# Kernel tuning notes

Hardware: AMD Instinct MI355X
Metric: run time of the kernel (lower is better)

## Reference

```python
import jax, jax.numpy as jnp
from jax import lax
import numpy as np

B, T, D, H, W = 256, 1024, 4, 64, 128

# Tsit5 Butcher tableau
C2, C3, C4, C5 = 0.161, 0.327, 0.9, 0.9800255409045097
A21 = 0.161
A31, A32 = -0.008480655492356989, 0.335480655492357
A41, A42, A43 = 2.8971530571054935, -6.359448489975075, 4.3622954328695815
A51, A52, A53, A54 = 5.325864828439257, -11.748883564062828, 7.4955393428898365, -0.09249506636175525
A61, A62, A63, A64, A65 = 5.86145544294642, -12.92096931784711, 8.159367898576159, -0.071584973281401, -0.028269050394068383
BW1, BW2, BW3, BW4, BW5, BW6 = 0.09646076681806523, 0.01, 0.4798896504144996, 1.379008574103742, -3.290069515436081, 2.324710524099774


def setup_inputs() -> dict:
    key = jax.random.key(0)
    ks = jax.random.split(key, 20)
    f32 = jnp.float32
    ts = jnp.arange(T, dtype=f32)
    coef = lambda k: 0.1 * jax.random.normal(k, (B, T - 1, D), f32)
    g = lambda k, shp, fan: jax.random.normal(k, shp, f32) / np.sqrt(fan)
    return {
        'ts': ts,
        'coef_d': coef(ks[0]), 'coef_c': coef(ks[1]),
        'coef_b': coef(ks[2]), 'coef_a': coef(ks[3]),
        # initial MLP: D -> W -> W -> H (softplus hidden, identity final)
        'W0': g(ks[4], (W, D), D), 'b0': jnp.zeros((W,), f32),
        'W1': g(ks[5], (W, W), W), 'b1': jnp.zeros((W,), f32),
        'W2': g(ks[6], (H, W), W), 'b2': jnp.zeros((H,), f32),
        # vector-field MLP: H -> W -> W -> H*D (softplus hidden, tanh final)
        'F0': g(ks[7], (W, H), H), 'g0': jnp.zeros((W,), f32),
        'F1': g(ks[8], (W, W), W), 'g1': jnp.zeros((W,), f32),
        'F2': g(ks[9], (H * D, W), W), 'g2': jnp.zeros((H * D,), f32),
        # readout: H -> 3
        'L': g(ks[10], (3, H), H), 'lb': jnp.zeros((3,), f32),
        'evolving_out': 1,
    }


def reference(ts, coef_d, coef_c, coef_b, coef_a,
              W0, b0, W1, b1, W2, b2,
              F0, g0, F1, g1, F2, g2, L, lb, evolving_out):
    sp = jax.nn.softplus

    def vf(y, dx):  # y: (B,H), dx: (B,D) -> f(y) @ dX/dt : (B,H)
        h1 = sp(y @ F0.T + g0)
        h2 = sp(h1 @ F1.T + g1)
        f = jnp.tanh(h2 @ F2.T + g2).reshape(-1, H, D)
        return jnp.einsum('bhd,bd->bh', f, dx)

    def step(y, inp):
        dt, cb, cc, cd = inp  # dt scalar; cb/cc/cd: (B,D) cubic coeffs of interval
        dx = lambda frac: cb + frac * (2.0 * cc + 3.0 * frac * cd)
        k1 = vf(y, dx(0.0))
        k2 = vf(y + dt * (A21 * k1), dx(C2 * dt))
        k3 = vf(y + dt * (A31 * k1 + A32 * k2), dx(C3 * dt))
        k4 = vf(y + dt * (A41 * k1 + A42 * k2 + A43 * k3), dx(C4 * dt))
        k5 = vf(y + dt * (A51 * k1 + A52 * k2 + A53 * k3 + A54 * k4), dx(C5 * dt))
        k6 = vf(y + dt * (A61 * k1 + A62 * k2 + A63 * k3 + A64 * k4 + A65 * k5), dx(dt))
        ynew = y + dt * (BW1 * k1 + BW2 * k2 + BW3 * k3 + BW4 * k4 + BW5 * k5 + BW6 * k6)
        return ynew, ynew

    # y0 = initial_mlp(X(t0)); X(t0) = coef_a at first interval (frac = 0)
    x0 = coef_a[:, 0]  # (B,D)
    h1 = sp(x0 @ W0.T + b0)
    h2 = sp(h1 @ W1.T + b1)
    y0 = h2 @ W2.T + b2  # (B,H)

    dts = ts[1:] - ts[:-1]  # (T-1,)
    xs = (dts, coef_b.transpose(1, 0, 2), coef_c.transpose(1, 0, 2), coef_d.transpose(1, 0, 2))
    ylast, ys = lax.scan(step, y0, xs)  # ys: (T-1,B,H)

    if evolving_out:
        ys_all = jnp.concatenate([y0[None], ys], axis=0)  # (T,B,H)
        return jnp.einsum('tbh,oh->bto', ys_all, L) + lb  # (B,T,3)
    return ylast @ L.T + lb  # (B,3)
```

## Files before the change

### kernel.cpp

```cpp
#include <hip/hip_runtime.h>

namespace {

constexpr int NB    = 256;
constexpr int NT    = 1024;
constexpr int NSTEP = NT - 1;
constexpr int D = 4, H = 64, W = 128;

constexpr float cAT[6][5] = {
    {0.f, 0.f, 0.f, 0.f, 0.f},
    {0.161f, 0.f, 0.f, 0.f, 0.f},
    {-0.008480655492356989f, 0.335480655492357f, 0.f, 0.f, 0.f},
    {2.8971530571054935f, -6.359448489975075f, 4.3622954328695815f, 0.f, 0.f},
    {5.325864828439257f, -11.748883564062828f, 7.4955393428898365f, -0.09249506636175525f, 0.f},
    {5.86145544294642f, -12.92096931784711f, 8.159367898576159f, -0.071584973281401f, -0.028269050394068383f}};
constexpr float cFR[6] = {0.0f, 0.161f, 0.327f, 0.9f, 0.9800255409045097f, 1.0f};
constexpr float cBW[6] = {0.09646076681806523f, 0.01f, 0.4798896504144996f,
                          1.379008574103742f, -3.290069515436081f, 2.324710524099774f};

__device__ __forceinline__ float softplus_f(float x) {
    float e = __expf(-fabsf(x));
    return fmaxf(x, 0.0f) + __logf(1.0f + e);
}
__device__ __forceinline__ float tanh_f(float x) {
    float e = __expf(2.0f * x);
    return 1.0f - __fdividef(2.0f, 1.0f + e);
}

template <int CTRL>
__device__ __forceinline__ float dppmv(float x) {
    return __int_as_float(__builtin_amdgcn_mov_dpp(__float_as_int(x), CTRL, 0xF, 0xF, true));
}

__device__ __forceinline__ int pY(int i)  { return (i >> 4) * 20 + (i & 15); }
__device__ __forceinline__ int p1i(int i) { return (i >> 5) * 36 + (i & 31); }
__device__ __forceinline__ int p2i(int i) { return (i >> 6) * 72 + (i & 63); }

__global__ __launch_bounds__(512, 2)
void cde_kernel(const float* __restrict__ ts,
                const float* __restrict__ coef_d,
                const float* __restrict__ coef_c,
                const float* __restrict__ coef_b,
                const float* __restrict__ coef_a,
                const float* __restrict__ W0, const float* __restrict__ b0,
                const float* __restrict__ W1, const float* __restrict__ b1,
                const float* __restrict__ W2, const float* __restrict__ b2,
                const float* __restrict__ F0, const float* __restrict__ g0,
                const float* __restrict__ F1, const float* __restrict__ g1,
                const float* __restrict__ F2, const float* __restrict__ g2,
                const float* __restrict__ Lm, const float* __restrict__ lb,
                float* __restrict__ out)
{
    const int b    = blockIdx.x;
    const int tid  = threadIdx.x;

    const int j12  = tid >> 2;
    const int q12  = tid & 3;
    const int j3   = tid >> 1;
    const int q3   = tid & 1;
    const int d3   = j3 & 3;
    const int hown = tid >> 3;

    __shared__ __align__(16) float s_ys[80];
    __shared__ __align__(16) float s_h1[144];
    __shared__ __align__(16) float s_h2[136];

    float wA[16];
    float wB[32];
    float wC[64];
    #pragma unroll
    for (int i = 0; i < 16; i += 4) {
        float4 v = *reinterpret_cast<const float4*>(F0 + j12 * H + q12 * 16 + i);
        wA[i+0]=v.x; wA[i+1]=v.y; wA[i+2]=v.z; wA[i+3]=v.w;
    }
    #pragma unroll
    for (int i = 0; i < 32; i += 4) {
        float4 v = *reinterpret_cast<const float4*>(F1 + j12 * W + q12 * 32 + i);
        wB[i+0]=v.x; wB[i+1]=v.y; wB[i+2]=v.z; wB[i+3]=v.w;
    }
    #pragma unroll
    for (int i = 0; i < 64; i += 4) {
        float4 v = *reinterpret_cast<const float4*>(F2 + j3 * W + q3 * 64 + i);
        wC[i+0]=v.x; wC[i+1]=v.y; wC[i+2]=v.z; wC[i+3]=v.w;
    }
    const float g0r = g0[j12];
    const float g1r = g1[j12];
    const float g2r = g2[j3];
    const float L0r = Lm[0*H + (tid & 63)];
    const float L1r = Lm[1*H + (tid & 63)];
    const float L2r = Lm[2*H + (tid & 63)];
    const float lb0 = lb[0], lb1 = lb[1], lb2 = lb[2];

    const float* pA  = s_ys + q12 * 20;
    const float* pB  = s_h1 + q12 * 36;
    const float* pC  = s_h2 + q3  * 72;
    float* pw1 = s_h1 + p1i(j12);
    float* pw2 = s_h2 + p2i(j12);
    float* pwy = s_ys + pY(hown);

    if (tid < W) {
        const float4 x0 = *reinterpret_cast<const float4*>(coef_a + (size_t)b * NSTEP * D);
        const float4 w  = *reinterpret_cast<const float4*>(W0 + tid * D);
        s_h1[p1i(tid)] = softplus_f(w.x*x0.x + w.y*x0.y + w.z*x0.z + w.w*x0.w + b0[tid]);
    }
    __syncthreads();
    if (tid < W) {
        float a = b1[tid];
        #pragma unroll
        for (int blk = 0; blk < 4; ++blk)
            #pragma unroll
            for (int i = 0; i < 8; ++i) {
                float4 wv = *reinterpret_cast<const float4*>(W1 + tid * W + blk * 32 + 4 * i);
                float4 hv = *reinterpret_cast<const float4*>(s_h1 + blk * 36 + 4 * i);
                a += wv.x*hv.x + wv.y*hv.y + wv.z*hv.z + wv.w*hv.w;
            }
        s_h2[p2i(tid)] = softplus_f(a);
    }
    __syncthreads();
    if (tid < H) {
        float a = b2[tid];
        #pragma unroll
        for (int blk = 0; blk < 2; ++blk)
            #pragma unroll
            for (int i = 0; i < 16; ++i) {
                float4 wv = *reinterpret_cast<const float4*>(W2 + tid * W + blk * 64 + 4 * i);
                float4 hv = *reinterpret_cast<const float4*>(s_h2 + blk * 72 + 4 * i);
                a += wv.x*hv.x + wv.y*hv.y + wv.z*hv.z + wv.w*hv.w;
            }
        s_ys[pY(tid)] = a;
    }
    __syncthreads();

    float y = s_ys[pY(hown)];

    auto project = [&](int tslot) {
        if (tid < 64) {
            float yv = s_ys[pY(tid)];
            float p0 = yv * L0r, p1 = yv * L1r, p2 = yv * L2r;
            #pragma unroll
            for (int off = 32; off >= 1; off >>= 1) {
                p0 += __shfl_xor(p0, off);
                p1 += __shfl_xor(p1, off);
                p2 += __shfl_xor(p2, off);
            }
            if (tid == 0) {
                float* dst = out + ((size_t)b * NT + tslot) * 3;
                dst[0] = p0 + lb0; dst[1] = p1 + lb1; dst[2] = p2 + lb2;
            }
        }
    };
    project(0);

    const float* cb_p = coef_b + (size_t)b * NSTEP * D + d3;
    const float* cc_p = coef_c + (size_t)b * NSTEP * D + d3;
    const float* cd_p = coef_d + (size_t)b * NSTEP * D + d3;

    for (int t = 0; t < NSTEP; ++t) {
        const float cbd = cb_p[t * D];
        const float ccd = cc_p[t * D];
        const float cdd = cd_p[t * D];
        const float dtv = ts[t + 1] - ts[t];

        float k[6];

        #pragma unroll
        for (int s = 0; s < 6; ++s) {
            float4 h0 = *reinterpret_cast<const float4*>(pA + 0);
            float4 h1 = *reinterpret_cast<const float4*>(pA + 4);
            float4 h2 = *reinterpret_cast<const float4*>(pA + 8);
            float4 h3 = *reinterpret_cast<const float4*>(pA + 12);
            float a1  = wA[0]*h0.x + wA[1]*h0.y + wA[2]*h0.z + wA[3]*h0.w
                      + wA[4]*h1.x + wA[5]*h1.y + wA[6]*h1.z + wA[7]*h1.w;
            float a1b = wA[8]*h2.x + wA[9]*h2.y + wA[10]*h2.z + wA[11]*h2.w
                      + wA[12]*h3.x + wA[13]*h3.y + wA[14]*h3.z + wA[15]*h3.w;
            float a1s = a1 + a1b;
            a1s += dppmv<0xB1>(a1s);
            a1s += dppmv<0x4E>(a1s);
            if (q12 == 0) *pw1 = softplus_f(a1s + g0r);
            __syncthreads();

            float a2 = 0.f, a2b = 0.f;
            #pragma unroll
            for (int c = 0; c < 8; c += 2) {
                float4 u0 = *reinterpret_cast<const float4*>(pB + 4 * c);
                float4 u1 = *reinterpret_cast<const float4*>(pB + 4 * c + 4);
                a2  += wB[4*c+0]*u0.x + wB[4*c+1]*u0.y + wB[4*c+2]*u0.z + wB[4*c+3]*u0.w;
                a2b += wB[4*c+4]*u1.x + wB[4*c+5]*u1.y + wB[4*c+6]*u1.z + wB[4*c+7]*u1.w;
            }
            float a2s = a2 + a2b;
            a2s += dppmv<0xB1>(a2s);
            a2s += dppmv<0x4E>(a2s);
            if (q12 == 0) *pw2 = softplus_f(a2s + g1r);
            __syncthreads();

            float a3 = 0.f, a3b = 0.f;
            #pragma unroll
            for (int c = 0; c < 16; c += 2) {
                float4 u0 = *reinterpret_cast<const float4*>(pC + 4 * c);
                float4 u1 = *reinterpret_cast<const float4*>(pC + 4 * c + 4);
                a3  += wC[4*c+0]*u0.x + wC[4*c+1]*u0.y + wC[4*c+2]*u0.z + wC[4*c+3]*u0.w;
                a3b += wC[4*c+4]*u1.x + wC[4*c+5]*u1.y + wC[4*c+6]*u1.z + wC[4*c+7]*u1.w;
            }
            float a3s = a3 + a3b;
            a3s += dppmv<0xB1>(a3s);
            const float f = tanh_f(a3s + g2r);

            const float frac = cFR[s] * dtv;
            const float dxd  = fmaf(frac, fmaf(3.0f * frac, cdd, 2.0f * ccd), cbd);
            float v = f * dxd;
            v += dppmv<0x4E>(v);
            v += dppmv<0x141>(v);
            k[s] = v;

            float ysn;
            if (s < 5) {
                float acc = 0.f;
                #pragma unroll
                for (int i = 0; i <= s; ++i) acc = fmaf(cAT[s+1][i], k[i], acc);
                ysn = fmaf(dtv, acc, y);
            } else {
                float acc = 0.f;
                #pragma unroll
                for (int i = 0; i < 6; ++i) acc = fmaf(cBW[i], k[i], acc);
                ysn = fmaf(dtv, acc, y);
            }
            if ((tid & 7) == 0) *pwy = ysn;
            __syncthreads();
        }

        y = s_ys[pY(hown)];

        project(t + 1);
    }
}

}

extern "C" void kernel_launch(void* const* d_in, const int* in_sizes, int n_in,
                              void* d_out, int out_size, void* d_ws, size_t ws_size,
                              hipStream_t stream) {
    const float* ts     = (const float*)d_in[0];
    const float* coef_d = (const float*)d_in[1];
    const float* coef_c = (const float*)d_in[2];
    const float* coef_b = (const float*)d_in[3];
    const float* coef_a = (const float*)d_in[4];
    const float* W0 = (const float*)d_in[5];
    const float* b0 = (const float*)d_in[6];
    const float* W1 = (const float*)d_in[7];
    const float* b1 = (const float*)d_in[8];
    const float* W2 = (const float*)d_in[9];
    const float* b2 = (const float*)d_in[10];
    const float* F0 = (const float*)d_in[11];
    const float* g0 = (const float*)d_in[12];
    const float* F1 = (const float*)d_in[13];
    const float* g1 = (const float*)d_in[14];
    const float* F2 = (const float*)d_in[15];
    const float* g2 = (const float*)d_in[16];
    const float* Lm = (const float*)d_in[17];
    const float* lb = (const float*)d_in[18];
    float* out = (float*)d_out;

    hipLaunchKernelGGL(cde_kernel, dim3(NB), dim3(512), 0, stream,
                       ts, coef_d, coef_c, coef_b, coef_a,
                       W0, b0, W1, b1, W2, b2,
                       F0, g0, F1, g1, F2, g2, Lm, lb, out);
}
```

Before: 6.908 ms.

## Repartition vector-field MLP across lanes with packed FMA and transpose-style DPP reduction

Reassigns work so that each thread computes partial dot products for four output neurons over a short slice of the input, instead of one neuron over a long slice. Each thread now reads fewer shared-memory vectors per layer. Partial sums are combined with a DPP butterfly that acts as a transpose-reduce over 16 lanes. The inner products use packed two-wide float FMAs, and the shared buffers are re-padded to match the new access pattern. In the last layer all four D components are handled in one thread, and the CDE coefficients are loaded as float4. This removes the cross-lane reduction over D, but adds redundant tanh work and more select/DPP instructions.

```diff
diff --git a/kernel.cpp b/kernel.cpp
--- a/kernel.cpp
+++ b/kernel.cpp
@@ -6,6 +6,8 @@
 constexpr int NT    = 1024;
 constexpr int NSTEP = NT - 1;
 constexpr int D = 4, H = 64, W = 128;
+
+typedef float v2f __attribute__((ext_vector_type(2)));
 
 constexpr float cAT[6][5] = {
     {0.f, 0.f, 0.f, 0.f, 0.f},
@@ -18,6 +20,8 @@
 constexpr float cBW[6] = {0.09646076681806523f, 0.01f, 0.4798896504144996f,
                           1.379008574103742f, -3.290069515436081f, 2.324710524099774f};
 
+#define PINF(x) asm volatile("" : "+v"(x))
+
 __device__ __forceinline__ float softplus_f(float x) {
     float e = __expf(-fabsf(x));
     return fmaxf(x, 0.0f) + __logf(1.0f + e);
@@ -32,9 +36,8 @@
     return __int_as_float(__builtin_amdgcn_mov_dpp(__float_as_int(x), CTRL, 0xF, 0xF, true));
 }
 
-__device__ __forceinline__ int pY(int i)  { return (i >> 4) * 20 + (i & 15); }
-__device__ __forceinline__ int p1i(int i) { return (i >> 5) * 36 + (i & 31); }
-__device__ __forceinline__ int p2i(int i) { return (i >> 6) * 72 + (i & 63); }
+__device__ __forceinline__ int p1m(int i) { return i + ((i >> 3) << 2); }
+__device__ __forceinline__ int p2m(int i) { return i + ((i >> 4) << 2); }
 
 __global__ __launch_bounds__(512, 2)
 void cde_kernel(const float* __restrict__ ts,
@@ -51,91 +54,126 @@
                 const float* __restrict__ Lm, const float* __restrict__ lb,
                 float* __restrict__ out)
 {
-    const int b    = blockIdx.x;
-    const int tid  = threadIdx.x;
-
-    const int j12  = tid >> 2;
-    const int q12  = tid & 3;
-    const int j3   = tid >> 1;
-    const int q3   = tid & 1;
-    const int d3   = j3 & 3;
-    const int hown = tid >> 3;
-
-    __shared__ __align__(16) float s_ys[80];
-    __shared__ __align__(16) float s_h1[144];
-    __shared__ __align__(16) float s_h2[136];
-
-    float wA[16];
-    float wB[32];
-    float wC[64];
-    #pragma unroll
-    for (int i = 0; i < 16; i += 4) {
-        float4 v = *reinterpret_cast<const float4*>(F0 + j12 * H + q12 * 16 + i);
-        wA[i+0]=v.x; wA[i+1]=v.y; wA[i+2]=v.z; wA[i+3]=v.w;
-    }
-    #pragma unroll
-    for (int i = 0; i < 32; i += 4) {
-        float4 v = *reinterpret_cast<const float4*>(F1 + j12 * W + q12 * 32 + i);
-        wB[i+0]=v.x; wB[i+1]=v.y; wB[i+2]=v.z; wB[i+3]=v.w;
-    }
-    #pragma unroll
-    for (int i = 0; i < 64; i += 4) {
-        float4 v = *reinterpret_cast<const float4*>(F2 + j3 * W + q3 * 64 + i);
-        wC[i+0]=v.x; wC[i+1]=v.y; wC[i+2]=v.z; wC[i+3]=v.w;
-    }
-    const float g0r = g0[j12];
-    const float g1r = g1[j12];
-    const float g2r = g2[j3];
-    const float L0r = Lm[0*H + (tid & 63)];
-    const float L1r = Lm[1*H + (tid & 63)];
-    const float L2r = Lm[2*H + (tid & 63)];
+    const int b   = blockIdx.x;
+    const int tid = threadIdx.x;
+
+    const int q1 = tid & 15;
+    const int gO = tid >> 4;
+    const int q3 = tid & 7;
+    const int g3 = tid >> 3;
+    const bool wr12 = (q1 < 4);
+    const bool wry  = (q3 == 0);
+    const bool pb0  = (tid & 1) != 0;
+    const bool pb1  = (tid & 2) != 0;
+
+    __shared__ __align__(16) float s_ys[64];
+    __shared__ __align__(16) float s_h1[192];
+    __shared__ __align__(16) float s_h2[160];
+
+    v2f wA2[8];
+    v2f wB2[16];
+    v2f wC2[32];
+    #pragma unroll
+    for (int j = 0; j < 4; ++j) {
+        float4 v = *reinterpret_cast<const float4*>(F0 + (4*gO + j) * H + 4*q1);
+        wA2[2*j]   = v2f{v.x, v.y};
+        wA2[2*j+1] = v2f{v.z, v.w};
+    }
+    #pragma unroll
+    for (int j = 0; j < 4; ++j)
+        #pragma unroll
+        for (int m = 0; m < 2; ++m) {
+            float4 v = *reinterpret_cast<const float4*>(F1 + (4*gO + j) * W + 8*q1 + 4*m);
+            wB2[4*j + 2*m]     = v2f{v.x, v.y};
+            wB2[4*j + 2*m + 1] = v2f{v.z, v.w};
+        }
+    #pragma unroll
+    for (int j = 0; j < 4; ++j)
+        #pragma unroll
+        for (int m = 0; m < 4; ++m) {
+            float4 v = *reinterpret_cast<const float4*>(F2 + (4*g3 + j) * W + 16*q3 + 4*m);
+            wC2[8*j + 2*m]     = v2f{v.x, v.y};
+            wC2[8*j + 2*m + 1] = v2f{v.z, v.w};
+        }
+    float g0w = g0[4*gO + (tid & 3)];
+    float g1w = g1[4*gO + (tid & 3)];
+    float g2v0 = g2[4*g3 + 0], g2v1 = g2[4*g3 + 1], g2v2 = g2[4*g3 + 2], g2v3 = g2[4*g3 + 3];
+    float L0r = Lm[0*H + (tid & 63)];
+    float L1r = Lm[1*H + (tid & 63)];
+    float L2r = Lm[2*H + (tid & 63)];
     const float lb0 = lb[0], lb1 = lb[1], lb2 = lb[2];
 
-    const float* pA  = s_ys + q12 * 20;
-    const float* pB  = s_h1 + q12 * 36;
-    const float* pC  = s_h2 + q3  * 72;
-    float* pw1 = s_h1 + p1i(j12);
-    float* pw2 = s_h2 + p2i(j12);
-    float* pwy = s_ys + pY(hown);
+    #pragma unroll
+    for (int i = 0; i < 8;  ++i) PINF(wA2[i]);
+    #pragma unroll
+    for (int i = 0; i < 16; ++i) PINF(wB2[i]);
+    #pragma unroll
+    for (int i = 0; i < 32; ++i) PINF(wC2[i]);
+    PINF(g0w); PINF(g1w); PINF(g2v0); PINF(g2v1); PINF(g2v2); PINF(g2v3);
+    PINF(L0r); PINF(L1r); PINF(L2r);
+
+    const float* pA = s_ys + 4*q1;
+    const float* pB = s_h1 + 12*q1;
+    const float* pC = s_h2 + 20*q3;
+    float* pw1 = s_h1 + p1m(4*gO + (tid & 3));
+    float* pw2 = s_h2 + p2m(4*gO + (tid & 3));
+    float* pwy = s_ys + g3;
+
+    auto reduce16 = [&](float v0, float v1, float v2, float v3) -> float {
+        v0 += dppmv<0x128>(v0); v1 += dppmv<0x128>(v1);
+        v2 += dppmv<0x128>(v2); v3 += dppmv<0x128>(v3);
+        v0 += dppmv<0x141>(v0); v1 += dppmv<0x141>(v1);
+        v2 += dppmv<0x141>(v2); v3 += dppmv<0x141>(v3);
+        float a  = pb0 ? v1 : v0;
+        float as = pb0 ? v0 : v1;
+        a += dppmv<0xB1>(as);
+        float c  = pb0 ? v3 : v2;
+        float cs = pb0 ? v2 : v3;
+        c += dppmv<0xB1>(cs);
+        float keep = pb1 ? c : a;
+        float send = pb1 ? a : c;
+        return keep + dppmv<0x4E>(send);
+    };
 
     if (tid < W) {
         const float4 x0 = *reinterpret_cast<const float4*>(coef_a + (size_t)b * NSTEP * D);
         const float4 w  = *reinterpret_cast<const float4*>(W0 + tid * D);
-        s_h1[p1i(tid)] = softplus_f(w.x*x0.x + w.y*x0.y + w.z*x0.z + w.w*x0.w + b0[tid]);
+        s_h1[p1m(tid)] = softplus_f(w.x*x0.x + w.y*x0.y + w.z*x0.z + w.w*x0.w + b0[tid]);
     }
     __syncthreads();
     if (tid < W) {
         float a = b1[tid];
         #pragma unroll
-        for (int blk = 0; blk < 4; ++blk)
-            #pragma unroll
-            for (int i = 0; i < 8; ++i) {
-                float4 wv = *reinterpret_cast<const float4*>(W1 + tid * W + blk * 32 + 4 * i);
-                float4 hv = *reinterpret_cast<const float4*>(s_h1 + blk * 36 + 4 * i);
-                a += wv.x*hv.x + wv.y*hv.y + wv.z*hv.z + wv.w*hv.w;
-            }
-        s_h2[p2i(tid)] = softplus_f(a);
+        for (int c = 0; c < 16; ++c) {
+            float4 wv0 = *reinterpret_cast<const float4*>(W1 + tid * W + 8*c);
+            float4 wv1 = *reinterpret_cast<const float4*>(W1 + tid * W + 8*c + 4);
+            float4 hv0 = *reinterpret_cast<const float4*>(s_h1 + 12*c);
+            float4 hv1 = *reinterpret_cast<const float4*>(s_h1 + 12*c + 4);
+            a += wv0.x*hv0.x + wv0.y*hv0.y + wv0.z*hv0.z + wv0.w*hv0.w
+               + wv1.x*hv1.x + wv1.y*hv1.y + wv1.z*hv1.z + wv1.w*hv1.w;
+        }
+        s_h2[p2m(tid)] = softplus_f(a);
     }
     __syncthreads();
     if (tid < H) {
         float a = b2[tid];
         #pragma unroll
-        for (int blk = 0; blk < 2; ++blk)
+        for (int c = 0; c < 8; ++c)
             #pragma unroll
-            for (int i = 0; i < 16; ++i) {
-                float4 wv = *reinterpret_cast<const float4*>(W2 + tid * W + blk * 64 + 4 * i);
-                float4 hv = *reinterpret_cast<const float4*>(s_h2 + blk * 72 + 4 * i);
+            for (int m = 0; m < 4; ++m) {
+                float4 wv = *reinterpret_cast<const float4*>(W2 + tid * W + 16*c + 4*m);
+                float4 hv = *reinterpret_cast<const float4*>(s_h2 + 20*c + 4*m);
                 a += wv.x*hv.x + wv.y*hv.y + wv.z*hv.z + wv.w*hv.w;
             }
-        s_ys[pY(tid)] = a;
+        s_ys[tid] = a;
     }
     __syncthreads();
 
-    float y = s_ys[pY(hown)];
+    float y = *pwy;
 
     auto project = [&](int tslot) {
         if (tid < 64) {
-            float yv = s_ys[pY(tid)];
+            float yv = s_ys[tid];
             float p0 = yv * L0r, p1 = yv * L1r, p2 = yv * L2r;
             #pragma unroll
             for (int off = 32; off >= 1; off >>= 1) {
@@ -151,85 +189,107 @@
     };
     project(0);
 
-    const float* cb_p = coef_b + (size_t)b * NSTEP * D + d3;
-    const float* cc_p = coef_c + (size_t)b * NSTEP * D + d3;
-    const float* cd_p = coef_d + (size_t)b * NSTEP * D + d3;
+    const float* cb_p = coef_b + (size_t)b * NSTEP * D;
+    const float* cc_p = coef_c + (size_t)b * NSTEP * D;
+    const float* cd_p = coef_d + (size_t)b * NSTEP * D;
 
     for (int t = 0; t < NSTEP; ++t) {
-        const float cbd = cb_p[t * D];
-        const float ccd = cc_p[t * D];
-        const float cdd = cd_p[t * D];
+        const float4 cb4 = *reinterpret_cast<const float4*>(cb_p + (size_t)t * D);
+        const float4 cc4 = *reinterpret_cast<const float4*>(cc_p + (size_t)t * D);
+        const float4 cd4 = *reinterpret_cast<const float4*>(cd_p + (size_t)t * D);
         const float dtv = ts[t + 1] - ts[t];
 
         float k[6];
 
         #pragma unroll
         for (int s = 0; s < 6; ++s) {
-            float4 h0 = *reinterpret_cast<const float4*>(pA + 0);
-            float4 h1 = *reinterpret_cast<const float4*>(pA + 4);
-            float4 h2 = *reinterpret_cast<const float4*>(pA + 8);
-            float4 h3 = *reinterpret_cast<const float4*>(pA + 12);
-            float a1  = wA[0]*h0.x + wA[1]*h0.y + wA[2]*h0.z + wA[3]*h0.w
-                      + wA[4]*h1.x + wA[5]*h1.y + wA[6]*h1.z + wA[7]*h1.w;
-            float a1b = wA[8]*h2.x + wA[9]*h2.y + wA[10]*h2.z + wA[11]*h2.w
-                      + wA[12]*h3.x + wA[13]*h3.y + wA[14]*h3.z + wA[15]*h3.w;
-            float a1s = a1 + a1b;
-            a1s += dppmv<0xB1>(a1s);
-            a1s += dppmv<0x4E>(a1s);
-            if (q12 == 0) *pw1 = softplus_f(a1s + g0r);
+            {
+                float4 hv = *reinterpret_cast<const float4*>(pA);
+                v2f h01 = v2f{hv.x, hv.y}, h23 = v2f{hv.z, hv.w};
+                v2f a0 = __builtin_elementwise_fma(wA2[1], h23, wA2[0] * h01);
+                v2f a1 = __builtin_elementwise_fma(wA2[3], h23, wA2[2] * h01);
+                v2f a2 = __builtin_elementwise_fma(wA2[5], h23, wA2[4] * h01);
+                v2f a3 = __builtin_elementwise_fma(wA2[7], h23, wA2[6] * h01);
+                float c = reduce16(a0.x + a0.y, a1.x + a1.y, a2.x + a2.y, a3.x + a3.y);
+                float sp = softplus_f(c + g0w);
+                if (wr12) *pw1 = sp;
+            }
             __syncthreads();
 
-            float a2 = 0.f, a2b = 0.f;
-            #pragma unroll
-            for (int c = 0; c < 8; c += 2) {
-                float4 u0 = *reinterpret_cast<const float4*>(pB + 4 * c);
-                float4 u1 = *reinterpret_cast<const float4*>(pB + 4 * c + 4);
-                a2  += wB[4*c+0]*u0.x + wB[4*c+1]*u0.y + wB[4*c+2]*u0.z + wB[4*c+3]*u0.w;
-                a2b += wB[4*c+4]*u1.x + wB[4*c+5]*u1.y + wB[4*c+6]*u1.z + wB[4*c+7]*u1.w;
-            }
-            float a2s = a2 + a2b;
-            a2s += dppmv<0xB1>(a2s);
-            a2s += dppmv<0x4E>(a2s);
-            if (q12 == 0) *pw2 = softplus_f(a2s + g1r);
+            {
+                float4 u0 = *reinterpret_cast<const float4*>(pB);
+                float4 u1 = *reinterpret_cast<const float4*>(pB + 4);
+                v2f h0 = v2f{u0.x, u0.y}, h1 = v2f{u0.z, u0.w};
+                v2f h2 = v2f{u1.x, u1.y}, h3 = v2f{u1.z, u1.w};
+                v2f a0 = wB2[0]*h0, a1 = wB2[4]*h0, a2 = wB2[8]*h0, a3 = wB2[12]*h0;
+                a0 = __builtin_elementwise_fma(wB2[1],  h1, a0);
+                a1 = __builtin_elementwise_fma(wB2[5],  h1, a1);
+                a2 = __builtin_elementwise_fma(wB2[9],  h1, a2);
+                a3 = __builtin_elementwise_fma(wB2[13], h1, a3);
+                a0 = __builtin_elementwise_fma(wB2[2],  h2, a0);
+                a1 = __builtin_elementwise_fma(wB2[6],  h2, a1);
+                a2 = __builtin_elementwise_fma(wB2[10], h2, a2);
+                a3 = __builtin_elementwise_fma(wB2[14], h2, a3);
+                a0 = __builtin_elementwise_fma(wB2[3],  h3, a0);
+                a1 = __builtin_elementwise_fma(wB2[7],  h3, a1);
+                a2 = __builtin_elementwise_fma(wB2[11], h3, a2);
+                a3 = __builtin_elementwise_fma(wB2[15], h3, a3);
+                float c = reduce16(a0.x + a0.y, a1.x + a1.y, a2.x + a2.y, a3.x + a3.y);
+                float sp = softplus_f(c + g1w);
+                if (wr12) *pw2 = sp;
+            }
             __syncthreads();
 
-            float a3 = 0.f, a3b = 0.f;
-            #pragma unroll
-            for (int c = 0; c < 16; c += 2) {
-                float4 u0 = *reinterpret_cast<const float4*>(pC + 4 * c);
-                float4 u1 = *reinterpret_cast<const float4*>(pC + 4 * c + 4);
-                a3  += wC[4*c+0]*u0.x + wC[4*c+1]*u0.y + wC[4*c+2]*u0.z + wC[4*c+3]*u0.w;
-                a3b += wC[4*c+4]*u1.x + wC[4*c+5]*u1.y + wC[4*c+6]*u1.z + wC[4*c+7]*u1.w;
-            }
-            float a3s = a3 + a3b;
-            a3s += dppmv<0xB1>(a3s);
-            const float f = tanh_f(a3s + g2r);
-
-            const float frac = cFR[s] * dtv;
-            const float dxd  = fmaf(frac, fmaf(3.0f * frac, cdd, 2.0f * ccd), cbd);
-            float v = f * dxd;
-            v += dppmv<0x4E>(v);
-            v += dppmv<0x141>(v);
-            k[s] = v;
-
-            float ysn;
-            if (s < 5) {
-                float acc = 0.f;
+            {
+                v2f a0 = v2f{0.f, 0.f}, a1 = a0, a2 = a0, a3 = a0;
                 #pragma unroll
-                for (int i = 0; i <= s; ++i) acc = fmaf(cAT[s+1][i], k[i], acc);
-                ysn = fmaf(dtv, acc, y);
-            } else {
-                float acc = 0.f;
-                #pragma unroll
-                for (int i = 0; i < 6; ++i) acc = fmaf(cBW[i], k[i], acc);
-                ysn = fmaf(dtv, acc, y);
-            }
-            if ((tid & 7) == 0) *pwy = ysn;
+                for (int m = 0; m < 4; ++m) {
+                    float4 u = *reinterpret_cast<const float4*>(pC + 4*m);
+                    v2f hlo = v2f{u.x, u.y}, hhi = v2f{u.z, u.w};
+                    a0 = __builtin_elementwise_fma(wC2[2*m],      hlo, a0);
+                    a0 = __builtin_elementwise_fma(wC2[2*m+1],    hhi, a0);
+                    a1 = __builtin_elementwise_fma(wC2[8+2*m],    hlo, a1);
+                    a1 = __builtin_elementwise_fma(wC2[8+2*m+1],  hhi, a1);
+                    a2 = __builtin_elementwise_fma(wC2[16+2*m],   hlo, a2);
+                    a2 = __builtin_elementwise_fma(wC2[16+2*m+1], hhi, a2);
+                    a3 = __builtin_elementwise_fma(wC2[24+2*m],   hlo, a3);
+                    a3 = __builtin_elementwise_fma(wC2[24+2*m+1], hhi, a3);
+                }
+                float v0 = a0.x + a0.y, v1 = a1.x + a1.y, v2 = a2.x + a2.y, v3 = a3.x + a3.y;
+                v0 += dppmv<0xB1>(v0); v1 += dppmv<0xB1>(v1); v2 += dppmv<0xB1>(v2); v3 += dppmv<0xB1>(v3);
+                v0 += dppmv<0x4E>(v0); v1 += dppmv<0x4E>(v1); v2 += dppmv<0x4E>(v2); v3 += dppmv<0x4E>(v3);
+                v0 += dppmv<0x141>(v0); v1 += dppmv<0x141>(v1); v2 += dppmv<0x141>(v2); v3 += dppmv<0x141>(v3);
+
+                const float f0 = tanh_f(v0 + g2v0);
+                const float f1 = tanh_f(v1 + g2v1);
+                const float f2 = tanh_f(v2 + g2v2);
+                const float f3 = tanh_f(v3 + g2v3);
+
+                const float frac = cFR[s] * dtv;
+                const float dx0 = fmaf(frac, fmaf(3.0f*frac, cd4.x, 2.0f*cc4.x), cb4.x);
+                const float dx1 = fmaf(frac, fmaf(3.0f*frac, cd4.y, 2.0f*cc4.y), cb4.y);
+                const float dx2 = fmaf(frac, fmaf(3.0f*frac, cd4.z, 2.0f*cc4.z), cb4.z);
+                const float dx3 = fmaf(frac, fmaf(3.0f*frac, cd4.w, 2.0f*cc4.w), cb4.w);
+                k[s] = fmaf(f0, dx0, fmaf(f1, dx1, fmaf(f2, dx2, f3 * dx3)));
+
+                float ysn;
+                if (s < 5) {
+                    float acc = 0.f;
+                    #pragma unroll
+                    for (int i = 0; i <= s; ++i) acc = fmaf(cAT[s+1][i], k[i], acc);
+                    ysn = fmaf(dtv, acc, y);
+                } else {
+                    float acc = 0.f;
+                    #pragma unroll
+                    for (int i = 0; i < 6; ++i) acc = fmaf(cBW[i], k[i], acc);
+                    ysn = fmaf(dtv, acc, y);
+                }
+                if (wry) *pwy = ysn;
+            }
             __syncthreads();
         }
 
-        y = s_ys[pY(hown)];
-
+        y = *pwy;
         project(t + 1);
     }
 }
```

Result: slower. 7.807 ms (+13.0%).

## Compute two output rows per thread in layers 2 and 3 to reuse shared loads

Applied to the files above, without the earlier changes.

Layers 2 and 3 of the vector-field MLP are remapped so each thread computes partial dot products for two output neurons over a shorter slice of the input. Each float4 read from shared memory is then used twice, which cuts LDS traffic per FMA. The cost is extra DPP reduction steps and a different lane-to-dimension mapping for the dX contraction, which now sums duplicate partials scaled by 0.5. Register count per thread stays about the same.

```diff
diff --git a/kernel.cpp b/kernel.cpp
--- a/kernel.cpp
+++ b/kernel.cpp
@@ -56,47 +56,53 @@
 
     const int j12  = tid >> 2;
     const int q12  = tid & 3;
-    const int j3   = tid >> 1;
-    const int q3   = tid & 1;
-    const int d3   = j3 & 3;
-    const int hown = tid >> 3;
+    const int og   = tid >> 3;
+    const int q2   = tid & 7;
+    const int grp  = tid >> 2;
+    const int qc   = tid & 3;
+    const int g3   = tid >> 3;
+    const int dsel = ((tid >> 2) & 1) * 2 + (tid & 1);
 
     __shared__ __align__(16) float s_ys[80];
     __shared__ __align__(16) float s_h1[144];
     __shared__ __align__(16) float s_h2[136];
 
     float wA[16];
-    float wB[32];
-    float wC[64];
+    float wB0[16], wB1[16];
+    float wC0[32], wC1[32];
     #pragma unroll
     for (int i = 0; i < 16; i += 4) {
         float4 v = *reinterpret_cast<const float4*>(F0 + j12 * H + q12 * 16 + i);
         wA[i+0]=v.x; wA[i+1]=v.y; wA[i+2]=v.z; wA[i+3]=v.w;
     }
     #pragma unroll
+    for (int i = 0; i < 16; i += 4) {
+        float4 v0 = *reinterpret_cast<const float4*>(F1 + (2*og)     * W + q2 * 16 + i);
+        float4 v1 = *reinterpret_cast<const float4*>(F1 + (2*og + 1) * W + q2 * 16 + i);
+        wB0[i+0]=v0.x; wB0[i+1]=v0.y; wB0[i+2]=v0.z; wB0[i+3]=v0.w;
+        wB1[i+0]=v1.x; wB1[i+1]=v1.y; wB1[i+2]=v1.z; wB1[i+3]=v1.w;
+    }
+    #pragma unroll
     for (int i = 0; i < 32; i += 4) {
-        float4 v = *reinterpret_cast<const float4*>(F1 + j12 * W + q12 * 32 + i);
-        wB[i+0]=v.x; wB[i+1]=v.y; wB[i+2]=v.z; wB[i+3]=v.w;
-    }
-    #pragma unroll
-    for (int i = 0; i < 64; i += 4) {
-        float4 v = *reinterpret_cast<const float4*>(F2 + j3 * W + q3 * 64 + i);
-        wC[i+0]=v.x; wC[i+1]=v.y; wC[i+2]=v.z; wC[i+3]=v.w;
+        float4 v0 = *reinterpret_cast<const float4*>(F2 + (2*grp)     * W + qc * 32 + i);
+        float4 v1 = *reinterpret_cast<const float4*>(F2 + (2*grp + 1) * W + qc * 32 + i);
+        wC0[i+0]=v0.x; wC0[i+1]=v0.y; wC0[i+2]=v0.z; wC0[i+3]=v0.w;
+        wC1[i+0]=v1.x; wC1[i+1]=v1.y; wC1[i+2]=v1.z; wC1[i+3]=v1.w;
     }
     const float g0r = g0[j12];
-    const float g1r = g1[j12];
-    const float g2r = g2[j3];
+    const float g1s = g1[2*og  + (q2  & 1)];
+    const float g2s = g2[2*grp + (tid & 1)];
     const float L0r = Lm[0*H + (tid & 63)];
     const float L1r = Lm[1*H + (tid & 63)];
     const float L2r = Lm[2*H + (tid & 63)];
     const float lb0 = lb[0], lb1 = lb[1], lb2 = lb[2];
 
-    const float* pA  = s_ys + q12 * 20;
-    const float* pB  = s_h1 + q12 * 36;
-    const float* pC  = s_h2 + q3  * 72;
+    const float* pA = s_ys + q12 * 20;
+    const float* pB = s_h1 + (q2 >> 1) * 36 + (q2 & 1) * 16;
+    const float* pC = s_h2 + (qc >> 1) * 72 + (qc & 1) * 32;
     float* pw1 = s_h1 + p1i(j12);
-    float* pw2 = s_h2 + p2i(j12);
-    float* pwy = s_ys + pY(hown);
+    float* pw2 = s_h2 + p2i(2*og + (q2 & 1));
+    float* pwy = s_ys + pY(g3);
 
     if (tid < W) {
         const float4 x0 = *reinterpret_cast<const float4*>(coef_a + (size_t)b * NSTEP * D);
@@ -131,7 +137,7 @@
     }
     __syncthreads();
 
-    float y = s_ys[pY(hown)];
+    float y = s_ys[pY(g3)];
 
     auto project = [&](int tslot) {
         if (tid < 64) {
@@ -151,85 +157,95 @@
     };
     project(0);
 
-    const float* cb_p = coef_b + (size_t)b * NSTEP * D + d3;
-    const float* cc_p = coef_c + (size_t)b * NSTEP * D + d3;
-    const float* cd_p = coef_d + (size_t)b * NSTEP * D + d3;
+    const float* cb_pl = coef_b + (size_t)b * NSTEP * D + dsel;
+    const float* cc_pl = coef_c + (size_t)b * NSTEP * D + dsel;
+    const float* cd_pl = coef_d + (size_t)b * NSTEP * D + dsel;
 
     for (int t = 0; t < NSTEP; ++t) {
-        const float cbd = cb_p[t * D];
-        const float ccd = cc_p[t * D];
-        const float cdd = cd_p[t * D];
+        const float cbd = cb_pl[(size_t)t * D];
+        const float ccd = cc_pl[(size_t)t * D];
+        const float cdd = cd_pl[(size_t)t * D];
         const float dtv = ts[t + 1] - ts[t];
 
         float k[6];
 
         #pragma unroll
         for (int s = 0; s < 6; ++s) {
-            float4 h0 = *reinterpret_cast<const float4*>(pA + 0);
-            float4 h1 = *reinterpret_cast<const float4*>(pA + 4);
-            float4 h2 = *reinterpret_cast<const float4*>(pA + 8);
-            float4 h3 = *reinterpret_cast<const float4*>(pA + 12);
-            float a1  = wA[0]*h0.x + wA[1]*h0.y + wA[2]*h0.z + wA[3]*h0.w
-                      + wA[4]*h1.x + wA[5]*h1.y + wA[6]*h1.z + wA[7]*h1.w;
-            float a1b = wA[8]*h2.x + wA[9]*h2.y + wA[10]*h2.z + wA[11]*h2.w
-                      + wA[12]*h3.x + wA[13]*h3.y + wA[14]*h3.z + wA[15]*h3.w;
-            float a1s = a1 + a1b;
-            a1s += dppmv<0xB1>(a1s);
-            a1s += dppmv<0x4E>(a1s);
-            if (q12 == 0) *pw1 = softplus_f(a1s + g0r);
+            {
+                float4 h0 = *reinterpret_cast<const float4*>(pA + 0);
+                float4 h1 = *reinterpret_cast<const float4*>(pA + 4);
+                float4 h2 = *reinterpret_cast<const float4*>(pA + 8);
+                float4 h3 = *reinterpret_cast<const float4*>(pA + 12);
+                float a1  = wA[0]*h0.x + wA[1]*h0.y + wA[2]*h0.z + wA[3]*h0.w
+                          + wA[4]*h1.x + wA[5]*h1.y + wA[6]*h1.z + wA[7]*h1.w;
+                float a1b = wA[8]*h2.x + wA[9]*h2.y + wA[10]*h2.z + wA[11]*h2.w
+                          + wA[12]*h3.x + wA[13]*h3.y + wA[14]*h3.z + wA[15]*h3.w;
+                float a1s = a1 + a1b;
+                a1s += dppmv<0xB1>(a1s);
+                a1s += dppmv<0x4E>(a1s);
+                if (q12 == 0) *pw1 = softplus_f(a1s + g0r);
+            }
             __syncthreads();
 
-            float a2 = 0.f, a2b = 0.f;
-            #pragma unroll
-            for (int c = 0; c < 8; c += 2) {
-                float4 u0 = *reinterpret_cast<const float4*>(pB + 4 * c);
-                float4 u1 = *reinterpret_cast<const float4*>(pB + 4 * c + 4);
-                a2  += wB[4*c+0]*u0.x + wB[4*c+1]*u0.y + wB[4*c+2]*u0.z + wB[4*c+3]*u0.w;
-                a2b += wB[4*c+4]*u1.x + wB[4*c+5]*u1.y + wB[4*c+6]*u1.z + wB[4*c+7]*u1.w;
-            }
-            float a2s = a2 + a2b;
-            a2s += dppmv<0xB1>(a2s);
-            a2s += dppmv<0x4E>(a2s);
-            if (q12 == 0) *pw2 = softplus_f(a2s + g1r);
+            {
+                float4 u0 = *reinterpret_cast<const float4*>(pB + 0);
+                float4 u1 = *reinterpret_cast<const float4*>(pB + 4);
+                float4 u2 = *reinterpret_cast<const float4*>(pB + 8);
+                float4 u3 = *reinterpret_cast<const float4*>(pB + 12);
+                float p0 = wB0[0]*u0.x + wB0[1]*u0.y + wB0[2]*u0.z + wB0[3]*u0.w
+                         + wB0[4]*u1.x + wB0[5]*u1.y + wB0[6]*u1.z + wB0[7]*u1.w
+                         + wB0[8]*u2.x + wB0[9]*u2.y + wB0[10]*u2.z + wB0[11]*u2.w
+                         + wB0[12]*u3.x + wB0[13]*u3.y + wB0[14]*u3.z + wB0[15]*u3.w;
+                float p1 = wB1[0]*u0.x + wB1[1]*u0.y + wB1[2]*u0.z + wB1[3]*u0.w
+                         + wB1[4]*u1.x + wB1[5]*u1.y + wB1[6]*u1.z + wB1[7]*u1.w
+                         + wB1[8]*u2.x + wB1[9]*u2.y + wB1[10]*u2.z + wB1[11]*u2.w
+                         + wB1[12]*u3.x + wB1[13]*u3.y + wB1[14]*u3.z + wB1[15]*u3.w;
+                p0 += dppmv<0xB1>(p0); p1 += dppmv<0xB1>(p1);
+                p0 += dppmv<0x4E>(p0); p1 += dppmv<0x4E>(p1);
+                p0 += dppmv<0x141>(p0); p1 += dppmv<0x141>(p1);
+                float spv = softplus_f(((q2 & 1) ? p1 : p0) + g1s);
+                if (q2 < 2) *pw2 = spv;
+            }
             __syncthreads();
 
-            float a3 = 0.f, a3b = 0.f;
-            #pragma unroll
-            for (int c = 0; c < 16; c += 2) {
-                float4 u0 = *reinterpret_cast<const float4*>(pC + 4 * c);
-                float4 u1 = *reinterpret_cast<const float4*>(pC + 4 * c + 4);
-                a3  += wC[4*c+0]*u0.x + wC[4*c+1]*u0.y + wC[4*c+2]*u0.z + wC[4*c+3]*u0.w;
-                a3b += wC[4*c+4]*u1.x + wC[4*c+5]*u1.y + wC[4*c+6]*u1.z + wC[4*c+7]*u1.w;
-            }
-            float a3s = a3 + a3b;
-            a3s += dppmv<0xB1>(a3s);
-            const float f = tanh_f(a3s + g2r);
-
-            const float frac = cFR[s] * dtv;
-            const float dxd  = fmaf(frac, fmaf(3.0f * frac, cdd, 2.0f * ccd), cbd);
-            float v = f * dxd;
-            v += dppmv<0x4E>(v);
-            v += dppmv<0x141>(v);
-            k[s] = v;
-
-            float ysn;
-            if (s < 5) {
-                float acc = 0.f;
+            {
+                float p0 = 0.f, p1 = 0.f;
                 #pragma unroll
-                for (int i = 0; i <= s; ++i) acc = fmaf(cAT[s+1][i], k[i], acc);
-                ysn = fmaf(dtv, acc, y);
-            } else {
-                float acc = 0.f;
-                #pragma unroll
-                for (int i = 0; i < 6; ++i) acc = fmaf(cBW[i], k[i], acc);
-                ysn = fmaf(dtv, acc, y);
-            }
-            if ((tid & 7) == 0) *pwy = ysn;
+                for (int m = 0; m < 8; ++m) {
+                    float4 u = *reinterpret_cast<const float4*>(pC + 4*m);
+                    p0 += wC0[4*m+0]*u.x + wC0[4*m+1]*u.y + wC0[4*m+2]*u.z + wC0[4*m+3]*u.w;
+                    p1 += wC1[4*m+0]*u.x + wC1[4*m+1]*u.y + wC1[4*m+2]*u.z + wC1[4*m+3]*u.w;
+                }
+                p0 += dppmv<0xB1>(p0); p1 += dppmv<0xB1>(p1);
+                p0 += dppmv<0x4E>(p0); p1 += dppmv<0x4E>(p1);
+                const float ft = tanh_f(((tid & 1) ? p1 : p0) + g2s);
+
+                const float frac = cFR[s] * dtv;
+                const float dxd  = fmaf(frac, fmaf(3.0f * frac, cdd, 2.0f * ccd), cbd);
+                float pk = ft * dxd * 0.5f;
+                pk += dppmv<0xB1>(pk);
+                pk += dppmv<0x4E>(pk);
+                pk += dppmv<0x141>(pk);
+                k[s] = pk;
+
+                float ysn;
+                if (s < 5) {
+                    float acc = 0.f;
+                    #pragma unroll
+                    for (int i = 0; i <= s; ++i) acc = fmaf(cAT[s+1][i], k[i], acc);
+                    ysn = fmaf(dtv, acc, y);
+                } else {
+                    float acc = 0.f;
+                    #pragma unroll
+                    for (int i = 0; i < 6; ++i) acc = fmaf(cBW[i], k[i], acc);
+                    ysn = fmaf(dtv, acc, y);
+                }
+                if ((tid & 7) == 0) *pwy = ysn;
+            }
             __syncthreads();
         }
 
-        y = s_ys[pY(hown)];
-
+        y = *pwy;
         project(t + 1);
     }
 }
```

After: 6.208 ms. -10.1%, faster.
